# Optimization experiments

Hardware: AMD Instinct MI355X
Metric: run time of the kernel (lower is better)

Reference implementation:

```python
import jax, jax.numpy as jnp
import numpy as np

N_BUILDINGS = 4096
NUM_CLUSTERS = 128
EMBED_DIM = 128
TEMPORAL_DIM = 24


def setup_inputs() -> dict:
    key = jax.random.key(0)
    ks = jax.random.split(key, 12)
    E, N, C, T = EMBED_DIM, N_BUILDINGS, NUM_CLUSTERS, TEMPORAL_DIM

    def lin(k, fi, fo):
        k1, k2 = jax.random.split(k)
        w = jax.random.normal(k1, (fo, fi), jnp.float32) / np.sqrt(fi).astype(np.float32)
        b = jax.random.normal(k2, (fo,), jnp.float32) * 0.01
        return w, b

    fp_w1, fp_b1 = lin(ks[0], 2 * E + 2, 128)
    fp_w2, fp_b2 = lin(ks[1], 128, 64)
    fp_w3, fp_b3 = lin(ks[2], 64, 1)
    en_w1, en_b1 = lin(ks[3], 1, 16)
    en_w2, en_b2 = lin(ks[4], 16, 1)
    ps_w1, ps_b1 = lin(ks[5], E, 32)
    ps_w2, ps_b2 = lin(ks[6], 32, 1)

    embeddings = jax.random.normal(ks[7], (1, N, E), jnp.float32)
    generation = jax.random.uniform(ks[8], (1, N, T), jnp.float32) * 50.0
    consumption = jax.random.uniform(ks[9], (1, N, T), jnp.float32) * 50.0
    positions = jax.random.uniform(ks[10], (1, N, 2), jnp.float32) * 1000.0
    cluster_assignments = (jnp.arange(N) % C)[None, :].astype(jnp.int32)

    return dict(embeddings=embeddings, generation=generation, consumption=consumption,
                positions=positions,
                fp_w1=fp_w1, fp_b1=fp_b1, fp_w2=fp_w2, fp_b2=fp_b2, fp_w3=fp_w3, fp_b3=fp_b3,
                en_w1=en_w1, en_b1=en_b1, en_w2=en_w2, en_b2=en_b2,
                ps_w1=ps_w1, ps_b1=ps_b1, ps_w2=ps_w2, ps_b2=ps_b2,
                cluster_assignments=cluster_assignments, num_clusters=C, current_hour=12)


def _greedy_cluster(net0, prio, effm, pf):
    """Greedy allocation within one cluster. net0,prio: [K]; effm,pf: [K,K].
    Surplus rows and deficit cols are both visited in descending priority order;
    non-surplus rows have avail=0 and non-deficit cols have needed<=0, matching the
    original code's subset selection + break/continue semantics."""
    K = net0.shape[0]
    order = jnp.argsort(-prio)
    inv = jnp.argsort(order)
    net_o = net0[order]
    eff_o = effm[order][:, order]
    pf_o = pf[order][:, order]

    def outer(dnet, i):
        avail0 = jnp.maximum(net_o[i], 0.0)  # surplus net is never mutated

        def inner(carry, j):
            avail, dn = carry
            needed = -dn[j]
            active = (avail > 0.0) & (needed > 0.0)
            f = jnp.where(active, jnp.minimum(jnp.minimum(avail, needed), pf_o[i, j]), 0.0)
            dn = dn.at[j].add(f * eff_o[i, j])  # deficit receives delivered flow
            return (avail - f, dn), (f, active)

        (_, dnet), (frow, arow) = jax.lax.scan(inner, (avail0, dnet), jnp.arange(K))
        return dnet, (frow, arow)

    dnet, (flows_o, act_o) = jax.lax.scan(outer, net_o, jnp.arange(K))
    return flows_o[inv][:, inv], act_o[inv][:, inv], dnet[inv]


def _forward(embeddings, generation, consumption, positions,
             fp_w1, fp_b1, fp_w2, fp_b2, fp_w3, fp_b3,
             en_w1, en_b1, en_w2, en_b2,
             ps_w1, ps_b1, ps_w2, ps_b2,
             cluster_assignments, num_clusters, current_hour):
    B, N, E = embeddings.shape
    C = num_clusters
    K = N // C
    net = generation[0, :, current_hour] - consumption[0, :, current_hour]  # [N]

    g = jnp.argsort(cluster_assignments[0]).reshape(C, K)  # [C,K] building ids per cluster
    emb_c = embeddings[0][g]   # [C,K,E]
    pos_c = positions[0][g]    # [C,K,2]
    net_c = net[g]             # [C,K]

    # priority scorer (eval mode)
    h = jax.nn.relu(emb_c @ ps_w1.T + ps_b1)
    prio_c = jax.nn.sigmoid(h @ ps_w2.T + ps_b2)[..., 0]  # [C,K]

    # pairwise distances within cluster
    dist = jnp.linalg.norm(pos_c[:, :, None, :] - pos_c[:, None, :, :], axis=-1)  # [C,K,K]

    # efficiency net: eff = 0.85 + 0.13*sigmoid(MLP(dist/1000))
    eh = jax.nn.relu((dist / 1000.0)[..., None] * en_w1[:, 0] + en_b1)  # [C,K,K,16]
    eff = 0.85 + 0.13 * jax.nn.sigmoid(eh @ en_w2.T + en_b2)[..., 0]    # [C,K,K]

    # flow predictor on concat([emb_i, emb_j, dist, hour/24]); split W1 to avoid
    # materializing the [C,K,K,2E+2] feature tensor. Dropout is eval-mode identity.
    W1a, W1b = fp_w1[:, :E], fp_w1[:, E:2 * E]
    w1d, w1h = fp_w1[:, 2 * E], fp_w1[:, 2 * E + 1]
    hi = emb_c @ W1a.T  # [C,K,128]
    hj = emb_c @ W1b.T  # [C,K,128]
    hour_f = current_hour / 24.0
    h1 = jax.nn.relu(hi[:, :, None, :] + hj[:, None, :, :] + dist[..., None] * w1d + hour_f * w1h + fp_b1)
    h2 = jax.nn.relu(h1 @ fp_w2.T + fp_b2)
    pflow = jax.nn.softplus(h2 @ fp_w3.T + fp_b3)[..., 0]  # [C,K,K]

    flows_c, act_c, dnet_c = jax.vmap(_greedy_cluster)(net_c, prio_c, eff, pflow)

    sharing = jnp.zeros((N, N), embeddings.dtype).at[g[:, :, None], g[:, None, :]].set(flows_c)
    effmat = jnp.ones((N, N), embeddings.dtype).at[g[:, :, None], g[:, None, :]].set(
        jnp.where(act_c, eff, 1.0))
    net_after = jnp.zeros((N,), embeddings.dtype).at[g].set(dnet_c)

    sharing = sharing[None]
    effmat = effmat[None]
    total_shared = sharing.sum()
    energy_sent = sharing.sum(axis=2)
    energy_received = (sharing * effmat).sum(axis=1)
    return sharing, effmat, total_shared, energy_sent, energy_received, net_after[None]


def reference(embeddings, generation, consumption, positions,
              fp_w1, fp_b1, fp_w2, fp_b2, fp_w3, fp_b3,
              en_w1, en_b1, en_w2, en_b2,
              ps_w1, ps_b1, ps_w2, ps_b2,
              cluster_assignments, num_clusters, current_hour):
    return _forward(embeddings, generation, consumption, positions,
                    fp_w1, fp_b1, fp_w2, fp_b2, fp_w3, fp_b3,
                    en_w1, en_b1, en_w2, en_b2,
                    ps_w1, ps_b1, ps_w2, ps_b2,
                    cluster_assignments, num_clusters, current_hour)
```

## Files before the change

kernel.cpp:

```cpp
#include <hip/hip_runtime.h>
#include <math.h>

#define NB 4096
#define NC 128
#define NK 32
#define NE 128

typedef __bf16 bf16x8 __attribute__((ext_vector_type(8)));
typedef float floatx4 __attribute__((ext_vector_type(4)));

__device__ __forceinline__ float sigmoidf_(float x){
  if (x >= 0.f){ float z = expf(-x); return 1.f/(1.f+z); }
  float z = expf(x); return z/(1.f+z);
}
__device__ __forceinline__ float softplusf_(float x){
  return fmaxf(x, 0.f) + log1pf(expf(-fabsf(x)));
}
__device__ __forceinline__ unsigned int pack_bf16(float a, float b){
  unsigned short ua = __builtin_bit_cast(unsigned short, (__bf16)a);
  unsigned short ub = __builtin_bit_cast(unsigned short, (__bf16)b);
  return (unsigned int)ua | ((unsigned int)ub << 16);
}

__global__ void k_hijprio(const float* __restrict__ emb, const float* __restrict__ gen,
                          const float* __restrict__ cons, const float* __restrict__ fp_w1,
                          const float* __restrict__ fp_b1, const float* __restrict__ fp_w2,
                          const float* __restrict__ ps_w1, const float* __restrict__ ps_b1,
                          const float* __restrict__ ps_w2, const float* __restrict__ ps_b2,
                          const int* __restrict__ assign, const int* __restrict__ hourp,
                          float* __restrict__ hi, float* __restrict__ hj,
                          float* __restrict__ net, float* __restrict__ prio,
                          int* __restrict__ g, int* __restrict__ row_of,
                          float* __restrict__ w1d_c, float* __restrict__ bzc,
                          uint4* __restrict__ w2f, float* __restrict__ total){
  int bid = blockIdx.x;
  int t = threadIdx.x;
  if (bid < 512){
    __shared__ float es[8*132];
    __shared__ float wsm[128*33];
    int i0 = bid*8;
    for (int idx = t; idx < 8*128; idx += 256){
      int b = idx >> 7, e = idx & 127;
      es[b*132 + e] = emb[(i0 + b)*128 + e];
    }
    for (int idx = t; idx < 4096; idx += 256){
      int q = idx >> 7, e = idx & 127;
      wsm[e*33 + q] = ps_w1[q*128 + e];
    }
    __syncthreads();
    {
      int o = t & 127, half = t >> 7;
      const float* w1r = fp_w1 + o*258;
      float ai[4], aj[4];
#pragma unroll
      for (int r = 0; r < 4; ++r){ ai[r] = 0.f; aj[r] = 0.f; }
      for (int e = 0; e < 128; e += 4){
        float wa0 = w1r[e+0], wa1 = w1r[e+1], wa2 = w1r[e+2], wa3 = w1r[e+3];
        float wb0 = w1r[128+e+0], wb1 = w1r[128+e+1], wb2 = w1r[128+e+2], wb3 = w1r[128+e+3];
#pragma unroll
        for (int r = 0; r < 4; ++r){
          float4 ev = *(const float4*)&es[(half*4 + r)*132 + e];
          ai[r] = fmaf(ev.x, wa0, fmaf(ev.y, wa1, fmaf(ev.z, wa2, fmaf(ev.w, wa3, ai[r]))));
          aj[r] = fmaf(ev.x, wb0, fmaf(ev.y, wb1, fmaf(ev.z, wb2, fmaf(ev.w, wb3, aj[r]))));
        }
      }
#pragma unroll
      for (int r = 0; r < 4; ++r){
        int b = i0 + half*4 + r;
        hi[b*128 + o] = ai[r];
        hj[b*128 + o] = aj[r];
      }
    }
    {
      int bl = t >> 5, q = t & 31;
      int i = i0 + bl;
      float acc = ps_b1[q];
      const float* er = &es[bl*132];
      for (int e = 0; e < 128; ++e) acc = fmaf(er[e], wsm[e*33 + q], acc);
      float v = fmaxf(acc, 0.f) * ps_w2[q];
      for (int m = 16; m >= 1; m >>= 1) v += __shfl_xor(v, m, 32);
      if (q == 0){
        prio[i] = sigmoidf_(v + ps_b2[0]);
        int h = hourp[0];
        net[i] = gen[i*24 + h] - cons[i*24 + h];
      }
    }
  } else if (bid < 528){
    __shared__ int hist[NC];
    __shared__ int loc[256];
    int start = (bid - 512)*256;
    for (int c = t; c < NC; c += 256) hist[c] = 0;
    __syncthreads();
    for (int j = t; j < start; j += 256) atomicAdd(&hist[assign[j]], 1);
    int i = start + t;
    int c = assign[i];
    loc[t] = c;
    __syncthreads();
    int r = hist[c];
    for (int j = 0; j < 256; ++j) r += (j < t && loc[j] == c) ? 1 : 0;
    if (r >= NK) r = NK - 1;
    g[c*NK + r] = i;
    row_of[i] = c*NK + r;
  } else if (bid == 528){
    if (t < 128){
      float hour_f = (float)hourp[0] / 24.0f;
      w1d_c[t] = fp_w1[t*258 + 256];
      bzc[t]   = fmaf(hour_f, fp_w1[t*258 + 257], fp_b1[t]);
    }
    if (t == 128) total[0] = 0.f;
  } else {
    for (int ff = t; ff < 1024; ff += 256){
      int lane = ff & 63, fi = ff >> 6;
      int nt = fi >> 2, ks = fi & 3;
      int o = nt*16 + (lane & 15);
      int kb = ks*32 + (lane >> 4)*8;
      const float* src = fp_w2 + o*128 + kb;
      uint4 u;
      u.x = pack_bf16(src[0], src[1]);
      u.y = pack_bf16(src[2], src[3]);
      u.z = pack_bf16(src[4], src[5]);
      u.w = pack_bf16(src[6], src[7]);
      w2f[ff] = u;
    }
  }
}

__global__ __launch_bounds__(256) void k_pfgreedy(
    const float* __restrict__ hi, const float* __restrict__ hj,
    const float* __restrict__ pos, const float* __restrict__ net,
    const float* __restrict__ prio, const float* __restrict__ w1d_c,
    const float* __restrict__ bzc, const uint4* __restrict__ w2f,
    const float* __restrict__ fp_b2, const float* __restrict__ fp_w3,
    const float* __restrict__ fp_b3, const float* __restrict__ en_w1,
    const float* __restrict__ en_b1, const float* __restrict__ en_w2,
    const float* __restrict__ en_b2, const int* __restrict__ g,
    float* __restrict__ fl_c, float* __restrict__ ef_c, float* __restrict__ total,
    float* __restrict__ esent, float* __restrict__ erecv, float* __restrict__ nafter){
  __shared__ float pf_s[1024];
  __shared__ float ef_s[1024];
  __shared__ float px[32], py[32];
  __shared__ int gl[32];
  __shared__ int order_s[32];
  int t = threadIdx.x;
  int lane = t & 63, wv = t >> 6;
  int c = blockIdx.x;
  if (t < 32){
    int b = g[c*NK + t];
    gl[t] = b;
    px[t] = pos[2*b];
    py[t] = pos[2*b + 1];
  }
  __syncthreads();
  {
    int l16 = lane & 15, quad = lane >> 4;
    bf16x8 bfr[4][4];
#pragma unroll
    for (int nt = 0; nt < 4; ++nt)
#pragma unroll
      for (int ks = 0; ks < 4; ++ks)
        bfr[nt][ks] = __builtin_bit_cast(bf16x8, w2f[(nt*4 + ks)*64 + lane]);
    float b2v[4], w3v[4];
#pragma unroll
    for (int nt = 0; nt < 4; ++nt){
      b2v[nt] = fp_b2[nt*16 + l16];
      w3v[nt] = fp_w3[nt*16 + l16];
    }
    float b3 = fp_b3[0];
    const float4* wd4 = (const float4*)w1d_c;
    const float4* bz4 = (const float4*)bzc;
    for (int it = 0; it < 16; ++it){
      int tile = it*4 + wv;
      int i = tile >> 1, j0 = (tile & 1)*16;
      int j = j0 + l16;
      float dx = px[i] - px[j], dy = py[i] - py[j];
      float d = sqrtf(fmaf(dx, dx, dy*dy));
      const float4* hi4 = (const float4*)(hi + gl[i]*128);
      const float4* hj4 = (const float4*)(hj + gl[j]*128);
      bf16x8 af[4];
#pragma unroll
      for (int ks = 0; ks < 4; ++ks){
        int q8 = ks*8 + quad*2;
        float4 a0 = hi4[q8], a1 = hi4[q8 + 1];
        float4 b0 = hj4[q8], b1 = hj4[q8 + 1];
        float4 w0 = wd4[q8], w1 = wd4[q8 + 1];
        float4 z0 = bz4[q8], z1 = bz4[q8 + 1];
        float v0 = fmaxf(a0.x + b0.x + fmaf(d, w0.x, z0.x), 0.f);
        float v1 = fmaxf(a0.y + b0.y + fmaf(d, w0.y, z0.y), 0.f);
        float v2 = fmaxf(a0.z + b0.z + fmaf(d, w0.z, z0.z), 0.f);
        float v3 = fmaxf(a0.w + b0.w + fmaf(d, w0.w, z0.w), 0.f);
        float v4 = fmaxf(a1.x + b1.x + fmaf(d, w1.x, z1.x), 0.f);
        float v5 = fmaxf(a1.y + b1.y + fmaf(d, w1.y, z1.y), 0.f);
        float v6 = fmaxf(a1.z + b1.z + fmaf(d, w1.z, z1.z), 0.f);
        float v7 = fmaxf(a1.w + b1.w + fmaf(d, w1.w, z1.w), 0.f);
        uint4 u;
        u.x = pack_bf16(v0, v1);
        u.y = pack_bf16(v2, v3);
        u.z = pack_bf16(v4, v5);
        u.w = pack_bf16(v6, v7);
        af[ks] = __builtin_bit_cast(bf16x8, u);
      }
      floatx4 acc[4];
#pragma unroll
      for (int nt = 0; nt < 4; ++nt){
        acc[nt] = (floatx4){0.f, 0.f, 0.f, 0.f};
#pragma unroll
        for (int ks = 0; ks < 4; ++ks)
          acc[nt] = __builtin_amdgcn_mfma_f32_16x16x32_bf16(af[ks], bfr[nt][ks], acc[nt], 0, 0, 0);
      }
#pragma unroll
      for (int r = 0; r < 4; ++r){
        float s = 0.f;
#pragma unroll
        for (int nt = 0; nt < 4; ++nt)
          s = fmaf(fmaxf(acc[nt][r] + b2v[nt], 0.f), w3v[nt], s);
#pragma unroll
        for (int m = 8; m >= 1; m >>= 1) s += __shfl_xor(s, m);
        if (l16 == 0)
          pf_s[i*32 + j0 + quad*4 + r] = softplusf_(s + b3);
      }
    }
  }
  for (int e = t; e < 1024; e += 256){
    int ii = e >> 5, jj = e & 31;
    float dx = px[ii] - px[jj], dy = py[ii] - py[jj];
    float d = sqrtf(fmaf(dx, dx, dy*dy));
    float ds = d * (1.0f/1000.0f);
    float acc = en_b2[0];
#pragma unroll
    for (int q = 0; q < 16; ++q)
      acc = fmaf(fmaxf(fmaf(ds, en_w1[q], en_b1[q]), 0.f), en_w2[q], acc);
    ef_s[e] = 0.85f + 0.13f*sigmoidf_(acc);
  }
  if (t < 64){
    int tl = t & 31;
    float pr = (t < 32) ? prio[gl[t]] : -1e30f;
    int rank = 0;
    for (int k = 0; k < 32; ++k){
      float pk = __shfl(pr, k, 32);
      rank += ((pk > pr) || (pk == pr && k < tl)) ? 1 : 0;
    }
    if (t < 32) order_s[rank] = t;
  }
  __syncthreads();
  if (t < 64){
    int tl = t & 31;
    int b = order_s[tl];
    float net0 = net[gl[b]];
    float dnet = net0;
    float recv = 0.f;
    float ctotal = 0.f;
    for (int i = 0; i < 32; ++i){
      int a = order_s[i];
      float av0 = fmaxf(__shfl(net0, i, 32), 0.f);
      float pf = pf_s[a*32 + b];
      float ef = ef_s[a*32 + b];
      float needed = -dnet;
      float m = (needed > 0.f) ? fminf(needed, pf) : 0.f;
      float s = m;
#pragma unroll
      for (int dd = 1; dd < 32; dd <<= 1){
        float u = __shfl_up(s, dd, 32);
        if (tl >= dd) s += u;
      }
      float Se = __shfl_up(s, 1, 32);
      if (tl == 0) Se = 0.f;
      float rprev = fmaxf(av0 - Se, 0.f);
      int act = (rprev > 0.f) && (needed > 0.f);
      float f = fminf(m, rprev);
      dnet = fmaf(f, ef, dnet);
      recv = fmaf(f, ef, recv);
      if (t < 32){
        fl_c[c*1024 + a*32 + b] = f;
        ef_c[c*1024 + a*32 + b] = act ? ef : 1.0f;
      }
      float rs = f;
      for (int mm = 16; mm >= 1; mm >>= 1) rs += __shfl_xor(rs, mm, 32);
      if (t == 0){ esent[gl[a]] = rs; ctotal += rs; }
    }
    if (t < 32){
      nafter[gl[b]] = dnet;
      erecv[gl[b]]  = recv;
    }
    if (t == 0) atomicAdd(total, ctotal);
  }
}

__global__ __launch_bounds__(256) void k_write(
    const float* __restrict__ fl_c, const float* __restrict__ ef_c,
    const int* __restrict__ g, const int* __restrict__ row_of,
    float* __restrict__ sharing, float* __restrict__ effm){
  __shared__ float rowS[4096];
  __shared__ float rowE[4096];
  __shared__ int   cols[32];
  __shared__ float vals[32];
  __shared__ float vale[32];
  int t = threadIdx.x;
  int r = blockIdx.x;
  int ra = row_of[r];
  int c = ra >> 5, a = ra & 31;
  if (t < 32){
    cols[t] = g[c*NK + t];
    vals[t] = fl_c[c*1024 + a*32 + t];
    vale[t] = ef_c[c*1024 + a*32 + t];
  }
  float4 z4 = make_float4(0.f, 0.f, 0.f, 0.f);
  float4 o4 = make_float4(1.f, 1.f, 1.f, 1.f);
  float4* s4 = (float4*)rowS;
  float4* e4 = (float4*)rowE;
#pragma unroll
  for (int q = 0; q < 4; ++q){ s4[t + 256*q] = z4; e4[t + 256*q] = o4; }
  __syncthreads();
  if (t < 32){ rowS[cols[t]] = vals[t]; rowE[cols[t]] = vale[t]; }
  __syncthreads();
  float4* gs = (float4*)(sharing + (long)r*NB);
  float4* ge = (float4*)(effm    + (long)r*NB);
#pragma unroll
  for (int q = 0; q < 4; ++q){ gs[t + 256*q] = s4[t + 256*q]; ge[t + 256*q] = e4[t + 256*q]; }
}

extern "C" void kernel_launch(void* const* d_in, const int* in_sizes, int n_in,
                              void* d_out, int out_size, void* d_ws, size_t ws_size,
                              hipStream_t stream){
  (void)in_sizes; (void)n_in; (void)out_size; (void)ws_size;
  const float* emb   = (const float*)d_in[0];
  const float* gen   = (const float*)d_in[1];
  const float* cons  = (const float*)d_in[2];
  const float* pos   = (const float*)d_in[3];
  const float* fp_w1 = (const float*)d_in[4];
  const float* fp_b1 = (const float*)d_in[5];
  const float* fp_w2 = (const float*)d_in[6];
  const float* fp_b2 = (const float*)d_in[7];
  const float* fp_w3 = (const float*)d_in[8];
  const float* fp_b3 = (const float*)d_in[9];
  const float* en_w1 = (const float*)d_in[10];
  const float* en_b1 = (const float*)d_in[11];
  const float* en_w2 = (const float*)d_in[12];
  const float* en_b2 = (const float*)d_in[13];
  const float* ps_w1 = (const float*)d_in[14];
  const float* ps_b1 = (const float*)d_in[15];
  const float* ps_w2 = (const float*)d_in[16];
  const float* ps_b2 = (const float*)d_in[17];
  const int*   assign = (const int*)d_in[18];
  const int*   hourp  = (const int*)d_in[20];

  char* ws = (char*)d_ws;
  int*   g      = (int*)  (ws + 0);
  int*   row_of = (int*)  (ws + 16384);
  float* net    = (float*)(ws + 32768);
  float* prio   = (float*)(ws + 49152);
  float* w1d_c  = (float*)(ws + 65536);
  float* bzc    = (float*)(ws + 66048);
  uint4* w2f    = (uint4*)(ws + 131072);
  float* hi     = (float*)(ws + 262144);
  float* hj     = (float*)(ws + 2359296);
  float* fl_c   = (float*)(ws + 4456448);
  float* ef_c   = (float*)(ws + 4980736);

  float* sharing = (float*)d_out;
  float* effm    = sharing + (long)NB*NB;
  float* total   = effm + (long)NB*NB;
  float* esent   = total + 1;
  float* erecv   = esent + NB;
  float* nafter  = erecv + NB;

  hipLaunchKernelGGL(k_hijprio, dim3(530), dim3(256), 0, stream,
                     emb, gen, cons, fp_w1, fp_b1, fp_w2, ps_w1, ps_b1, ps_w2, ps_b2,
                     assign, hourp, hi, hj, net, prio, g, row_of, w1d_c, bzc, w2f, total);
  hipLaunchKernelGGL(k_pfgreedy, dim3(128), dim3(256), 0, stream,
                     hi, hj, pos, net, prio, w1d_c, bzc, w2f, fp_b2, fp_w3, fp_b3,
                     en_w1, en_b1, en_w2, en_b2, g,
                     fl_c, ef_c, total, esent, erecv, nafter);
  hipLaunchKernelGGL(k_write, dim3(4096), dim3(256), 0, stream,
                     fl_c, ef_c, g, row_of, sharing, effm);
}
```

Before: 262.6 us.

## Stage fp_w1 in LDS, widen pfgreedy block, buffer greedy outputs, nontemporal stores

```diff
diff --git a/kernel.cpp b/kernel.cpp
--- a/kernel.cpp
+++ b/kernel.cpp
@@ -38,6 +38,8 @@
   if (bid < 512){
     __shared__ float es[8*132];
     __shared__ float wsm[128*33];
+    __shared__ float wa_s[128*33];
+    __shared__ float wb_s[128*33];
     int i0 = bid*8;
     for (int idx = t; idx < 8*128; idx += 256){
       int b = idx >> 7, e = idx & 127;
@@ -47,16 +49,26 @@
       int q = idx >> 7, e = idx & 127;
       wsm[e*33 + q] = ps_w1[q*128 + e];
     }
-    __syncthreads();
-    {
-      int o = t & 127, half = t >> 7;
-      const float* w1r = fp_w1 + o*258;
-      float ai[4], aj[4];
-#pragma unroll
-      for (int r = 0; r < 4; ++r){ ai[r] = 0.f; aj[r] = 0.f; }
-      for (int e = 0; e < 128; e += 4){
-        float wa0 = w1r[e+0], wa1 = w1r[e+1], wa2 = w1r[e+2], wa3 = w1r[e+3];
-        float wb0 = w1r[128+e+0], wb1 = w1r[128+e+1], wb2 = w1r[128+e+2], wb3 = w1r[128+e+3];
+    int o = t & 127, half = t >> 7;
+    float ai[4], aj[4];
+#pragma unroll
+    for (int r = 0; r < 4; ++r){ ai[r] = 0.f; aj[r] = 0.f; }
+    for (int ch = 0; ch < 4; ++ch){
+      int ec = ch << 5;
+      if (ch) __syncthreads();
+      for (int idx = t; idx < 4096; idx += 256){
+        int row = idx >> 5, e2 = idx & 31;
+        wa_s[row*33 + e2] = fp_w1[row*258 + ec + e2];
+        wb_s[row*33 + e2] = fp_w1[row*258 + 128 + ec + e2];
+      }
+      __syncthreads();
+      const float* war = &wa_s[o*33];
+      const float* wbr = &wb_s[o*33];
+#pragma unroll
+      for (int e2 = 0; e2 < 32; e2 += 4){
+        float wa0 = war[e2+0], wa1 = war[e2+1], wa2 = war[e2+2], wa3 = war[e2+3];
+        float wb0 = wbr[e2+0], wb1 = wbr[e2+1], wb2 = wbr[e2+2], wb3 = wbr[e2+3];
+        int e = ec + e2;
 #pragma unroll
         for (int r = 0; r < 4; ++r){
           float4 ev = *(const float4*)&es[(half*4 + r)*132 + e];
@@ -64,12 +76,12 @@
           aj[r] = fmaf(ev.x, wb0, fmaf(ev.y, wb1, fmaf(ev.z, wb2, fmaf(ev.w, wb3, aj[r]))));
         }
       }
-#pragma unroll
-      for (int r = 0; r < 4; ++r){
-        int b = i0 + half*4 + r;
-        hi[b*128 + o] = ai[r];
-        hj[b*128 + o] = aj[r];
-      }
+    }
+#pragma unroll
+    for (int r = 0; r < 4; ++r){
+      int b = i0 + half*4 + r;
+      hi[b*128 + o] = ai[r];
+      hj[b*128 + o] = aj[r];
     }
     {
       int bl = t >> 5, q = t & 31;
@@ -125,7 +137,7 @@
   }
 }
 
-__global__ __launch_bounds__(256) void k_pfgreedy(
+__global__ __launch_bounds__(512) void k_pfgreedy(
     const float* __restrict__ hi, const float* __restrict__ hj,
     const float* __restrict__ pos, const float* __restrict__ net,
     const float* __restrict__ prio, const float* __restrict__ w1d_c,
@@ -138,6 +150,8 @@
     float* __restrict__ esent, float* __restrict__ erecv, float* __restrict__ nafter){
   __shared__ float pf_s[1024];
   __shared__ float ef_s[1024];
+  __shared__ float fl_s[1024];
+  __shared__ float efa_s[1024];
   __shared__ float px[32], py[32];
   __shared__ int gl[32];
   __shared__ int order_s[32];
@@ -168,8 +182,8 @@
     float b3 = fp_b3[0];
     const float4* wd4 = (const float4*)w1d_c;
     const float4* bz4 = (const float4*)bzc;
-    for (int it = 0; it < 16; ++it){
-      int tile = it*4 + wv;
+    for (int it = 0; it < 8; ++it){
+      int tile = it*8 + wv;
       int i = tile >> 1, j0 = (tile & 1)*16;
       int j = j0 + l16;
       float dx = px[i] - px[j], dy = py[i] - py[j];
@@ -220,7 +234,7 @@
       }
     }
   }
-  for (int e = t; e < 1024; e += 256){
+  for (int e = t; e < 1024; e += 512){
     int ii = e >> 5, jj = e & 31;
     float dx = px[ii] - px[jj], dy = py[ii] - py[jj];
     float d = sqrtf(fmaf(dx, dx, dy*dy));
@@ -248,7 +262,6 @@
     float net0 = net[gl[b]];
     float dnet = net0;
     float recv = 0.f;
-    float ctotal = 0.f;
     for (int i = 0; i < 32; ++i){
       int a = order_s[i];
       float av0 = fmaxf(__shfl(net0, i, 32), 0.f);
@@ -270,18 +283,29 @@
       dnet = fmaf(f, ef, dnet);
       recv = fmaf(f, ef, recv);
       if (t < 32){
-        fl_c[c*1024 + a*32 + b] = f;
-        ef_c[c*1024 + a*32 + b] = act ? ef : 1.0f;
-      }
-      float rs = f;
-      for (int mm = 16; mm >= 1; mm >>= 1) rs += __shfl_xor(rs, mm, 32);
-      if (t == 0){ esent[gl[a]] = rs; ctotal += rs; }
+        fl_s[a*32 + b]  = f;
+        efa_s[a*32 + b] = act ? ef : 1.0f;
+      }
     }
     if (t < 32){
       nafter[gl[b]] = dnet;
       erecv[gl[b]]  = recv;
     }
-    if (t == 0) atomicAdd(total, ctotal);
+  }
+  __syncthreads();
+  for (int e = t; e < 1024; e += 512){
+    fl_c[c*1024 + e] = fl_s[e];
+    ef_c[c*1024 + e] = efa_s[e];
+  }
+  if (t < 32){
+    float rs = 0.f;
+#pragma unroll
+    for (int j = 0; j < 32; ++j)
+      rs += fl_s[t*32 + ((j + t) & 31)];
+    esent[gl[t]] = rs;
+    float cs = rs;
+    for (int m = 16; m >= 1; m >>= 1) cs += __shfl_xor(cs, m, 32);
+    if (t == 0) atomicAdd(total, cs);
   }
 }
 
@@ -312,10 +336,15 @@
   __syncthreads();
   if (t < 32){ rowS[cols[t]] = vals[t]; rowE[cols[t]] = vale[t]; }
   __syncthreads();
-  float4* gs = (float4*)(sharing + (long)r*NB);
-  float4* ge = (float4*)(effm    + (long)r*NB);
-#pragma unroll
-  for (int q = 0; q < 4; ++q){ gs[t + 256*q] = s4[t + 256*q]; ge[t + 256*q] = e4[t + 256*q]; }
+  const floatx4* s4v = (const floatx4*)rowS;
+  const floatx4* e4v = (const floatx4*)rowE;
+  floatx4* gs = (floatx4*)(sharing + (long)r*NB);
+  floatx4* ge = (floatx4*)(effm    + (long)r*NB);
+#pragma unroll
+  for (int q = 0; q < 4; ++q){
+    __builtin_nontemporal_store(s4v[t + 256*q], &gs[t + 256*q]);
+    __builtin_nontemporal_store(e4v[t + 256*q], &ge[t + 256*q]);
+  }
 }
 
 extern "C" void kernel_launch(void* const* d_in, const int* in_sizes, int n_in,
@@ -366,7 +395,7 @@
   hipLaunchKernelGGL(k_hijprio, dim3(530), dim3(256), 0, stream,
                      emb, gen, cons, fp_w1, fp_b1, fp_w2, ps_w1, ps_b1, ps_w2, ps_b2,
                      assign, hourp, hi, hj, net, prio, g, row_of, w1d_c, bzc, w2f, total);
-  hipLaunchKernelGGL(k_pfgreedy, dim3(128), dim3(256), 0, stream,
+  hipLaunchKernelGGL(k_pfgreedy, dim3(128), dim3(512), 0, stream,
                      hi, hj, pos, net, prio, w1d_c, bzc, w2f, fp_b2, fp_w3, fp_b3,
                      en_w1, en_b1, en_w2, en_b2, g,
                      fl_c, ef_c, total, esent, erecv, nafter);
```

Result: faster. 256.4 us (-2.4%).
